# Kernel optimization log

Hardware: AMD Instinct MI355X
Metric: run time of the kernel (lower is better)

The kernel has to match this reference:

```python
import jax, jax.numpy as jnp
import numpy as np

B, T, E, H, S = 4, 4096, 1024, 16, 64
D = E // H  # head_dim = 64
ROPE_BASE = 10000.0


def _rotate_half(x):
    # interleaved rotate: out[..., 2i] = -x[..., 2i+1]; out[..., 2i+1] = x[..., 2i]
    x1 = x[..., ::2]
    x2 = x[..., 1::2]
    return jnp.stack([-x2, x1], axis=-1).reshape(x.shape)


def _rope_cos_sin(t, d):
    inv_freq = 1.0 / (ROPE_BASE ** (jnp.arange(0, d, 2, dtype=jnp.float32) / d))
    freqs = jnp.arange(t, dtype=jnp.float32)[:, None] * inv_freq[None, :]  # [t, d/2]
    emb = jnp.concatenate([freqs, freqs], axis=-1)  # [t, d]
    # broadcast over batch and heads for q/k of shape [b, t, h, d]
    return jnp.cos(emb)[None, :, None, :], jnp.sin(emb)[None, :, None, :]


def setup_inputs() -> dict:
    key = jax.random.key(0)
    ks = jax.random.split(key, 6)
    s = E ** -0.5
    return {
        "x": jax.random.normal(ks[0], (B, T, E), dtype=jnp.float32),
        "Wq": jax.random.normal(ks[1], (E, E), dtype=jnp.float32) * s,
        "Wk": jax.random.normal(ks[2], (E, E), dtype=jnp.float32) * s,
        "Wv": jax.random.normal(ks[3], (E, E), dtype=jnp.float32) * s,
        "Wout": jax.random.normal(ks[4], (E, E), dtype=jnp.float32) * s,
        "slot_keys": jax.random.normal(ks[5], (H, S, D), dtype=jnp.float32) * (D ** -0.5),
    }


def reference(x, Wq, Wk, Wv, Wout, slot_keys):
    b, t, e = x.shape
    h, s_slots, d = slot_keys.shape
    scale = d ** -0.5

    q = (x @ Wq.T).reshape(b, t, h, d)
    k = (x @ Wk.T).reshape(b, t, h, d)
    v = (x @ Wv.T).reshape(b, t, h, d)

    cos, sin = _rope_cos_sin(t, d)
    q = q * cos + _rotate_half(q) * sin
    k = k * cos + _rotate_half(k) * sin

    # write pass: route each token's value into memory slots
    write_logits = jnp.einsum('bthd,hsd->bths', k, slot_keys) * scale
    write_weights = jax.nn.softmax(write_logits, axis=-1)  # write_temperature = 1.0
    slot_state = jnp.einsum('bths,bthd->bshd', write_weights, v) / t

    # read pass: query the slot memory
    read_logits = jnp.einsum('bthd,bshd->bths', q, slot_state) * scale
    read_weights = jax.nn.softmax(read_logits, axis=-1)  # read_temperature = 1.0
    read_out = jnp.einsum('bths,bshd->bthd', read_weights, slot_state)

    return read_out.reshape(b, t, e) @ Wout.T
```

## Files before the change

kernel.cpp:

```cpp
#include <hip/hip_runtime.h>
#include <cstdint>
#include <cstddef>

#define BB 4
#define TT 4096
#define EE 1024
#define HH 16
#define SSLOTS 64
#define DD 64
#define MM (BB*TT)

typedef unsigned short u16;
typedef __attribute__((ext_vector_type(8))) short s16x8;
typedef __attribute__((ext_vector_type(4))) float f32x4;
typedef __attribute__((ext_vector_type(8))) unsigned short us8v;
typedef __attribute__((ext_vector_type(4))) unsigned short us4v;

#define MFMA16(a, b, c) __builtin_amdgcn_mfma_f32_16x16x32_bf16((a), (b), (c), 0, 0, 0)

__device__ __forceinline__ u16 f2bf(float x) {
  union { float f; uint32_t u; } c; c.f = x;
  uint32_t u = c.u;
  u += 0x7fffu + ((u >> 16) & 1u);
  return (u16)(u >> 16);
}

__device__ __forceinline__ float bf2f(u16 x) {
  union { uint32_t u; float f; } c; c.u = ((uint32_t)x) << 16;
  return c.f;
}

__device__ __forceinline__ void async16(const void* g, void* l) {
  auto lp = reinterpret_cast<__attribute__((address_space(3))) void*>(
      reinterpret_cast<uintptr_t>(l));
  auto gp = reinterpret_cast<const __attribute__((address_space(1))) void*>(
      reinterpret_cast<uintptr_t>(g));
  __builtin_amdgcn_global_load_lds(gp, lp, 16, 0, 0);
}

__device__ __forceinline__ us8v rope8(us8v kv, const float* __restrict__ rcp,
                                      const float* __restrict__ rsp) {
  float4 ca = *(const float4*)rcp;
  float4 cb = *(const float4*)(rcp + 4);
  float4 sa = *(const float4*)rsp;
  float4 sb = *(const float4*)(rsp + 4);
  float c[8] = {ca.x, ca.y, ca.z, ca.w, cb.x, cb.y, cb.z, cb.w};
  float s[8] = {sa.x, sa.y, sa.z, sa.w, sb.x, sb.y, sb.z, sb.w};
  float e[8];
#pragma unroll
  for (int m = 0; m < 8; ++m) e[m] = bf2f((u16)kv[m]);
  us8v o;
#pragma unroll
  for (int j = 0; j < 4; ++j) {
    o[2 * j]     = f2bf(e[2 * j] * c[2 * j]     - e[2 * j + 1] * s[2 * j]);
    o[2 * j + 1] = f2bf(e[2 * j + 1] * c[2 * j + 1] + e[2 * j] * s[2 * j + 1]);
  }
  return o;
}

__global__ __launch_bounds__(256) void k_prep(const float* __restrict__ x,
                                              const float* __restrict__ w0,
                                              const float* __restrict__ w1,
                                              const float* __restrict__ w2,
                                              const float* __restrict__ w3,
                                              u16* __restrict__ x16,
                                              u16* __restrict__ dW,
                                              u16* __restrict__ dWo,
                                              float* __restrict__ rc,
                                              float* __restrict__ rs) {
  int bid = blockIdx.x;
  if (bid < 16384) {
    int i = (bid * 256 + threadIdx.x) * 4;
    float4 v = *(const float4*)(x + i);
    us4v o = { f2bf(v.x), f2bf(v.y), f2bf(v.z), f2bf(v.w) };
    *(us4v*)(x16 + i) = o;
  } else if (bid < 16384 + 4096) {
    int bb = bid - 16384;
    int sel = bb >> 10;
    const float* s = (sel == 0) ? w0 : (sel == 1) ? w1 : (sel == 2) ? w2 : w3;
    u16* d = (sel < 3) ? (dW + (size_t)sel * EE * EE) : dWo;
    int i = ((bb & 1023) * 256 + threadIdx.x) * 4;
    float4 v = *(const float4*)(s + i);
    us4v o = { f2bf(v.x), f2bf(v.y), f2bf(v.z), f2bf(v.w) };
    *(us4v*)(d + i) = o;
  } else {
    int i = (bid - 16384 - 4096) * 256 + threadIdx.x;
    int t = i >> 5, f = i & 31;
    double invf = pow(10000.0, -(double)(2 * f) / 64.0);
    double th = fmod((double)t * invf, 6.28318530717958647692528676655900577);
    rc[i] = (float)cos(th);
    rs[i] = (float)sin(th);
  }
}


__device__ __forceinline__ void mm16(f32x4 (&acc)[8][4], const s16x8* a,
                                     const s16x8* b, int ab) {
#pragma unroll
  for (int im = 0; im < 4; ++im)
#pragma unroll
    for (int in = 0; in < 4; ++in)
      acc[ab + im][in] = MFMA16(a[im], b[in], acc[ab + im][in]);
}

__device__ __forceinline__ void gemm256(const u16* __restrict__ A,
                                        const u16* __restrict__ B,
                                        char* smem, f32x4 (&acc)[8][4]) {
  const int tid = threadIdx.x, lane = tid & 63, wave = tid >> 6;
  const int l16 = lane & 15, q4 = lane >> 4;
  const int wrow = (wave >> 2) * 128;
  const int wcol = (wave & 3) * 64;

  const int sr0 = wave * 32 + (lane >> 2);
  const int sr1 = sr0 + 16;
  const int sc  = (lane & 3) * 16;
  const size_t ga0 = (size_t)sr0 * 2048 + (size_t)(sc ^ (((sr0 >> 1) & 3) << 4));
  const size_t ga1 = (size_t)sr1 * 2048 + (size_t)(sc ^ (((sr1 >> 1) & 3) << 4));
  const int lo0 = sr0 * 64 + sc;
  const int lo1 = sr1 * 64 + sc;
  const char* Ab = (const char*)A;
  const char* Bb = (const char*)B;

  int offA[8], offB[4];
#pragma unroll
  for (int f = 0; f < 8; ++f) {
    int r = wrow + f * 16 + l16;
    offA[f] = (r * 64 + q4 * 16) ^ (((r >> 1) & 3) << 4);
  }
#pragma unroll
  for (int f = 0; f < 4; ++f) {
    int r = wcol + f * 16 + l16;
    offB[f] = (r * 64 + q4 * 16) ^ (((r >> 1) & 3) << 4);
  }

#define STG(dst, srcb, kb) do { \
    async16((srcb) + (size_t)(kb) + ga0, (dst) + lo0); \
    async16((srcb) + (size_t)(kb) + ga1, (dst) + lo1); } while (0)

  STG(smem +     0, Ab, 0);
  STG(smem + 32768, Bb, 0);
  STG(smem + 16384, Ab, 64);
  STG(smem + 49152, Bb, 64);
  STG(smem + 65536 +     0, Ab, 128);
  STG(smem + 65536 + 32768, Bb, 128);
  asm volatile("s_waitcnt vmcnt(4)" ::: "memory");
  __builtin_amdgcn_s_barrier();

  for (int tau = 0; tau < 16; ++tau) {
    char* cb = smem + ((tau & 1) << 16);
    char* nb = smem + (((tau + 1) & 1) << 16);
    const char* Ak0 = cb;
    const char* Ak1 = cb + 16384;
    const char* Bk0 = cb + 32768;
    const char* Bk1 = cb + 49152;
    const int kb1 = (tau + 1) << 7;
    const int kb2 = (tau + 2) << 7;
    const bool st1 = tau < 15, st2 = tau < 14;

    s16x8 a[4], b[4];

#pragma unroll
    for (int f = 0; f < 4; ++f) a[f] = *(const s16x8*)(Ak0 + offA[f]);
#pragma unroll
    for (int f = 0; f < 4; ++f) b[f] = *(const s16x8*)(Bk0 + offB[f]);
    if (st1) STG(nb + 16384, Ab, kb1 + 64);
    __builtin_amdgcn_s_barrier();
    asm volatile("s_waitcnt lgkmcnt(0)" ::: "memory");
    __builtin_amdgcn_s_setprio(1);
    mm16(acc, a, b, 0);
    __builtin_amdgcn_s_setprio(0);
    __builtin_amdgcn_s_barrier();

#pragma unroll
    for (int f = 0; f < 4; ++f) a[f] = *(const s16x8*)(Ak0 + offA[4 + f]);
    if (st1) STG(nb + 49152, Bb, kb1 + 64);
    if (st2) asm volatile("s_waitcnt vmcnt(6)" ::: "memory");
    else     asm volatile("s_waitcnt vmcnt(0)" ::: "memory");
    __builtin_amdgcn_s_barrier();
    asm volatile("s_waitcnt lgkmcnt(0)" ::: "memory");
    __builtin_amdgcn_s_setprio(1);
    mm16(acc, a, b, 4);
    __builtin_amdgcn_s_setprio(0);
    __builtin_amdgcn_s_barrier();

#pragma unroll
    for (int f = 0; f < 4; ++f) a[f] = *(const s16x8*)(Ak1 + offA[f]);
#pragma unroll
    for (int f = 0; f < 4; ++f) b[f] = *(const s16x8*)(Bk1 + offB[f]);
    if (st2) STG(cb, Ab, kb2);
    __builtin_amdgcn_s_barrier();
    asm volatile("s_waitcnt lgkmcnt(0)" ::: "memory");
    __builtin_amdgcn_s_setprio(1);
    mm16(acc, a, b, 0);
    __builtin_amdgcn_s_setprio(0);
    __builtin_amdgcn_s_barrier();

#pragma unroll
    for (int f = 0; f < 4; ++f) a[f] = *(const s16x8*)(Ak1 + offA[4 + f]);
    if (st2) STG(cb + 32768, Bb, kb2);
    if (st2) asm volatile("s_waitcnt vmcnt(6)" ::: "memory");
    else     asm volatile("s_waitcnt vmcnt(0)" ::: "memory");
    __builtin_amdgcn_s_barrier();
    asm volatile("s_waitcnt lgkmcnt(0)" ::: "memory");
    __builtin_amdgcn_s_setprio(1);
    mm16(acc, a, b, 4);
    __builtin_amdgcn_s_setprio(0);
    __builtin_amdgcn_s_barrier();
  }
#undef STG
}

__global__ __launch_bounds__(512, 2) void k_gemm_qkv(const u16* __restrict__ A,
                                                     const u16* __restrict__ Bw,
                                                     u16* __restrict__ q16,
                                                     u16* __restrict__ k16,
                                                     u16* __restrict__ v16) {
  __shared__ char smem[131072];
  const int bid = blockIdx.x;
  const int xcd = bid & 7, local = bid >> 3;
  const int mt = xcd * 8 + (local & 7);
  const int nt = local >> 3;
  const int m0 = mt * 256, n0 = nt * 256;

  f32x4 acc[8][4];
#pragma unroll
  for (int i = 0; i < 8; ++i)
#pragma unroll
    for (int j = 0; j < 4; ++j) acc[i][j] = (f32x4){0.f, 0.f, 0.f, 0.f};

  gemm256(A + (size_t)m0 * 1024, Bw + (size_t)n0 * 1024, smem, acc);

  const int tid = threadIdx.x, lane = tid & 63, wave = tid >> 6;
  const int l16 = lane & 15, q4 = lane >> 4;
  const int wrow = (wave >> 2) * 128, wn = (wave & 3) * 64;
  const int which = n0 >> 10;
  const int nbl = n0 & 1023;
  u16* dst = (which == 0) ? q16 : ((which == 1) ? k16 : v16);

#pragma unroll
  for (int im = 0; im < 8; ++im)
#pragma unroll
    for (int in = 0; in < 4; ++in)
#pragma unroll
      for (int reg = 0; reg < 4; ++reg) {
        float v = acc[im][in][reg];
        int m = m0 + wrow + im * 16 + q4 * 4 + reg;
        int nn = nbl + wn + in * 16 + l16;
        int bq = m >> 12, t = m & 4095;
        int h = nn >> 6, d = nn & 63;
        dst[((size_t)(bq * HH + h) * TT + t) * 64 + d] = f2bf(v);
      }
}

__global__ __launch_bounds__(512, 2) void k_gemm_out(const u16* __restrict__ A,
                                                     const u16* __restrict__ Bw,
                                                     float* __restrict__ C) {
  __shared__ char smem[131072];
  const int bid = blockIdx.x;
  const int xcd = bid & 7, local = bid >> 3;
  const int mt = xcd * 8 + (local & 7);
  const int nt = local >> 3;
  const int m0 = mt * 256, n0 = nt * 256;

  f32x4 acc[8][4];
#pragma unroll
  for (int i = 0; i < 8; ++i)
#pragma unroll
    for (int j = 0; j < 4; ++j) acc[i][j] = (f32x4){0.f, 0.f, 0.f, 0.f};

  gemm256(A + (size_t)m0 * 1024, Bw + (size_t)n0 * 1024, smem, acc);

  const int tid = threadIdx.x, lane = tid & 63, wave = tid >> 6;
  const int l16 = lane & 15, q4 = lane >> 4;
  const int wrow = (wave >> 2) * 128, wn = (wave & 3) * 64;
#pragma unroll
  for (int im = 0; im < 8; ++im)
#pragma unroll
    for (int in = 0; in < 4; ++in)
#pragma unroll
      for (int reg = 0; reg < 4; ++reg) {
        int m = m0 + wrow + im * 16 + q4 * 4 + reg;
        int n = n0 + wn + in * 16 + l16;
        C[(size_t)m * 1024 + n] = acc[im][in][reg];
      }
}

__global__ __launch_bounds__(256) void k_stage2(const u16* __restrict__ K16g,
                                                const u16* __restrict__ V16g,
                                                const float* __restrict__ SKg,
                                                const float* __restrict__ rc,
                                                const float* __restrict__ rs,
                                                float* __restrict__ SSb) {
  const int tid = threadIdx.x, lane = tid & 63, wave = tid >> 6;
  const int l16 = lane & 15, q4 = lane >> 4, q8 = q4 * 8;
  const int bh = blockIdx.x >> 4, tb = blockIdx.x & 15;
  const int h = bh & 15;

  __shared__ u16 Ks[128 * 88];
  __shared__ u16 Vs[64 * 136];
  __shared__ u16 SKs[64 * 88];
  u16* ww = Ks;

  const float* skh = SKg + (size_t)h * (SSLOTS * DD);
  for (int i = tid * 4; i < 4096; i += 1024) {
    float4 v = *(const float4*)(skh + i);
    us4v o = { f2bf(v.x), f2bf(v.y), f2bf(v.z), f2bf(v.w) };
    *(us4v*)&SKs[(i >> 6) * 88 + (i & 63)] = o;
  }

  f32x4 a2[4];
#pragma unroll
  for (int in = 0; in < 4; ++in) a2[in] = (f32x4){0.f, 0.f, 0.f, 0.f};

  const int w32 = wave * 32;
  for (int cc = 0; cc < 2; ++cc) {
    const int tg0 = tb * 256 + cc * 128;
    __syncthreads();

    const u16* ks = K16g + ((size_t)bh * TT + tg0) * 64;
    for (int idx = tid; idx < 1024; idx += 256) {
      int t = idx >> 3, p = idx & 7;
      us8v kv = *(const us8v*)(ks + (size_t)t * 64 + p * 8);
      int fi = (tg0 + t) * 32 + ((p * 8) & 31);
      us8v kr = rope8(kv, rc + fi, rs + fi);
      *(us8v*)&Ks[t * 88 + p * 8] = kr;
    }
    const u16* vsrc = V16g + ((size_t)bh * TT + tg0) * 64;
    for (int idx = tid; idx < 1024; idx += 256) {
      int t = idx & 127, dg = idx >> 7;
      us8v vv = *(const us8v*)(vsrc + (size_t)t * 64 + dg * 8);
#pragma unroll
      for (int j = 0; j < 8; ++j) Vs[(dg * 8 + j) * 136 + t] = vv[j];
    }
    __syncthreads();

    f32x4 a1[2][4];
#pragma unroll
    for (int im = 0; im < 2; ++im)
#pragma unroll
      for (int in = 0; in < 4; ++in) a1[im][in] = (f32x4){0.f, 0.f, 0.f, 0.f};
#pragma unroll
    for (int ksx = 0; ksx < 2; ++ksx) {
      s16x8 afr0 = *(const s16x8*)&Ks[(w32 + l16) * 88 + ksx * 32 + q8];
      s16x8 afr1 = *(const s16x8*)&Ks[(w32 + 16 + l16) * 88 + ksx * 32 + q8];
#pragma unroll
      for (int in = 0; in < 4; ++in) {
        s16x8 bfr = *(const s16x8*)&SKs[(in * 16 + l16) * 88 + ksx * 32 + q8];
        a1[0][in] = MFMA16(afr0, bfr, a1[0][in]);
        a1[1][in] = MFMA16(afr1, bfr, a1[1][in]);
      }
    }
    __syncthreads();

#pragma unroll
    for (int im = 0; im < 2; ++im)
#pragma unroll
      for (int reg = 0; reg < 4; ++reg) {
        float v0 = a1[im][0][reg] * 0.125f, v1 = a1[im][1][reg] * 0.125f;
        float v2 = a1[im][2][reg] * 0.125f, v3 = a1[im][3][reg] * 0.125f;
        float mx = fmaxf(fmaxf(v0, v1), fmaxf(v2, v3));
#pragma unroll
        for (int m = 1; m < 16; m <<= 1) mx = fmaxf(mx, __shfl_xor(mx, m));
        float e0 = __expf(v0 - mx), e1 = __expf(v1 - mx);
        float e2 = __expf(v2 - mx), e3 = __expf(v3 - mx);
        float sm = e0 + e1 + e2 + e3;
#pragma unroll
        for (int m = 1; m < 16; m <<= 1) sm += __shfl_xor(sm, m);
        float inv = 1.0f / sm;
        int tl = w32 + im * 16 + q4 * 4 + reg;
        ww[(l16) * 136 + tl]      = f2bf(e0 * inv);
        ww[(16 + l16) * 136 + tl] = f2bf(e1 * inv);
        ww[(32 + l16) * 136 + tl] = f2bf(e2 * inv);
        ww[(48 + l16) * 136 + tl] = f2bf(e3 * inv);
      }
    __syncthreads();

#pragma unroll
    for (int ksx = 0; ksx < 4; ++ksx) {
      s16x8 afr = *(const s16x8*)&ww[(wave * 16 + l16) * 136 + ksx * 32 + q8];
#pragma unroll
      for (int in = 0; in < 4; ++in) {
        s16x8 bfr = *(const s16x8*)&Vs[(in * 16 + l16) * 136 + ksx * 32 + q8];
        a2[in] = MFMA16(afr, bfr, a2[in]);
      }
    }
  }

  const float invT = 1.0f / (float)TT;
#pragma unroll
  for (int in = 0; in < 4; ++in)
#pragma unroll
    for (int reg = 0; reg < 4; ++reg) {
      int s = wave * 16 + q4 * 4 + reg;
      int d = in * 16 + l16;
      atomicAdd(&SSb[(size_t)bh * 4096 + s * 64 + d], a2[in][reg] * invT);
    }
}

__global__ __launch_bounds__(256) void k_stage3(const u16* __restrict__ Q16g,
                                                const float* __restrict__ SSg,
                                                const float* __restrict__ rc,
                                                const float* __restrict__ rs,
                                                u16* __restrict__ RO) {
  const int tid = threadIdx.x, lane = tid & 63, wave = tid >> 6;
  const int l16 = lane & 15, q4 = lane >> 4, q8 = q4 * 8;
  const int bh = blockIdx.x >> 5, ck = blockIdx.x & 31;
  const int b = bh >> 4, h = bh & 15;
  const int tg0 = ck * 128;

  __shared__ u16 Qs[128 * 88];
  __shared__ u16 ss_sd[64 * 88];
  __shared__ u16 ss_ds[64 * 88];
  u16* RWs = Qs;

  const float* ssp = SSg + (size_t)bh * 4096;
  for (int i = tid * 4; i < 4096; i += 1024) {
    float4 v = *(const float4*)(ssp + i);
    us4v o = { f2bf(v.x), f2bf(v.y), f2bf(v.z), f2bf(v.w) };
    int s = i >> 6, d = i & 63;
    *(us4v*)&ss_sd[s * 88 + d] = o;
    ss_ds[(d + 0) * 88 + s] = o[0];
    ss_ds[(d + 1) * 88 + s] = o[1];
    ss_ds[(d + 2) * 88 + s] = o[2];
    ss_ds[(d + 3) * 88 + s] = o[3];
  }
  const u16* qsrc = Q16g + ((size_t)bh * TT + tg0) * 64;
  for (int idx = tid; idx < 1024; idx += 256) {
    int t = idx >> 3, p = idx & 7;
    us8v qv = *(const us8v*)(qsrc + (size_t)t * 64 + p * 8);
    int fi = (tg0 + t) * 32 + ((p * 8) & 31);
    us8v qr = rope8(qv, rc + fi, rs + fi);
    *(us8v*)&Qs[t * 88 + p * 8] = qr;
  }
  __syncthreads();

  const int w32 = wave * 32;
  f32x4 a3[2][4];
#pragma unroll
  for (int i = 0; i < 2; ++i)
#pragma unroll
    for (int j = 0; j < 4; ++j) a3[i][j] = (f32x4){0.f, 0.f, 0.f, 0.f};
#pragma unroll
  for (int ksx = 0; ksx < 2; ++ksx) {
    s16x8 afr[2];
#pragma unroll
    for (int im = 0; im < 2; ++im)
      afr[im] = *(const s16x8*)&Qs[(w32 + im * 16 + l16) * 88 + ksx * 32 + q8];
#pragma unroll
    for (int in = 0; in < 4; ++in) {
      s16x8 bfr = *(const s16x8*)&ss_sd[(in * 16 + l16) * 88 + ksx * 32 + q8];
#pragma unroll
      for (int im = 0; im < 2; ++im) a3[im][in] = MFMA16(afr[im], bfr, a3[im][in]);
    }
  }
  __syncthreads();

#pragma unroll
  for (int im = 0; im < 2; ++im)
#pragma unroll
    for (int reg = 0; reg < 4; ++reg) {
      float v0 = a3[im][0][reg] * 0.125f, v1 = a3[im][1][reg] * 0.125f;
      float v2 = a3[im][2][reg] * 0.125f, v3 = a3[im][3][reg] * 0.125f;
      float mx = fmaxf(fmaxf(v0, v1), fmaxf(v2, v3));
#pragma unroll
      for (int m = 1; m < 16; m <<= 1) mx = fmaxf(mx, __shfl_xor(mx, m));
      float e0 = __expf(v0 - mx), e1 = __expf(v1 - mx);
      float e2 = __expf(v2 - mx), e3 = __expf(v3 - mx);
      float sm = e0 + e1 + e2 + e3;
#pragma unroll
      for (int m = 1; m < 16; m <<= 1) sm += __shfl_xor(sm, m);
      float inv = 1.0f / sm;
      int tl = w32 + im * 16 + q4 * 4 + reg;
      RWs[tl * 88 + l16]      = f2bf(e0 * inv);
      RWs[tl * 88 + 16 + l16] = f2bf(e1 * inv);
      RWs[tl * 88 + 32 + l16] = f2bf(e2 * inv);
      RWs[tl * 88 + 48 + l16] = f2bf(e3 * inv);
    }
  __syncthreads();

  f32x4 a4[2][4];
#pragma unroll
  for (int i = 0; i < 2; ++i)
#pragma unroll
    for (int j = 0; j < 4; ++j) a4[i][j] = (f32x4){0.f, 0.f, 0.f, 0.f};
#pragma unroll
  for (int ksx = 0; ksx < 2; ++ksx) {
    s16x8 afr[2];
#pragma unroll
    for (int im = 0; im < 2; ++im)
      afr[im] = *(const s16x8*)&RWs[(w32 + im * 16 + l16) * 88 + ksx * 32 + q8];
#pragma unroll
    for (int in = 0; in < 4; ++in) {
      s16x8 bfr = *(const s16x8*)&ss_ds[(in * 16 + l16) * 88 + ksx * 32 + q8];
#pragma unroll
      for (int im = 0; im < 2; ++im) a4[im][in] = MFMA16(afr[im], bfr, a4[im][in]);
    }
  }

#pragma unroll
  for (int im = 0; im < 2; ++im)
#pragma unroll
    for (int in = 0; in < 4; ++in)
#pragma unroll
      for (int reg = 0; reg < 4; ++reg) {
        int t = tg0 + w32 + im * 16 + q4 * 4 + reg;
        int d = in * 16 + l16;
        RO[((size_t)b * TT + t) * 1024 + h * 64 + d] = f2bf(a4[im][in][reg]);
      }
}

extern "C" void kernel_launch(void* const* d_in, const int* in_sizes, int n_in,
                              void* d_out, int out_size, void* d_ws, size_t ws_size,
                              hipStream_t stream) {
  const float* x  = (const float*)d_in[0];
  const float* Wq = (const float*)d_in[1];
  const float* Wk = (const float*)d_in[2];
  const float* Wv = (const float*)d_in[3];
  const float* Wo = (const float*)d_in[4];
  const float* SK = (const float*)d_in[5];
  float* out = (float*)d_out;

  char* w = (char*)d_ws;
  u16* x16 = (u16*)w;   w += (size_t)MM * EE * 2;
  u16* W16 = (u16*)w;   w += (size_t)3 * EE * EE * 2;
  u16* Wo16 = (u16*)w;  w += (size_t)EE * EE * 2;
  u16* Q16 = (u16*)w;   w += (size_t)BB * HH * TT * DD * 2;
  u16* K16 = (u16*)w;   w += (size_t)BB * HH * TT * DD * 2;
  u16* V16 = (u16*)w;   w += (size_t)BB * HH * TT * DD * 2;
  float* SSb = (float*)w; w += (size_t)BB * HH * SSLOTS * DD * 4;
  float* rc = (float*)w;  w += (size_t)TT * 32 * 4;
  float* rs = (float*)w;  w += (size_t)TT * 32 * 4;
  u16* RO16 = x16;

  if ((size_t)(w - (char*)d_ws) > ws_size) return;

  k_prep<<<16384 + 4096 + 512, 256, 0, stream>>>(x, Wq, Wk, Wv, Wo, x16, W16, Wo16, rc, rs);

  k_gemm_qkv<<<768, 512, 0, stream>>>(x16, W16, Q16, K16, V16);

  hipMemsetAsync(SSb, 0, (size_t)BB * HH * SSLOTS * DD * 4, stream);
  k_stage2<<<1024, 256, 0, stream>>>(K16, V16, SK, rc, rs, SSb);
  k_stage3<<<2048, 256, 0, stream>>>(Q16, SSb, rc, rs, RO16);

  k_gemm_out<<<256, 512, 0, stream>>>(RO16, Wo16, out);
}
```

Measured before the change: 346.5 us.

## Merge GEMM k-substeps into full-tile MFMA phases and replace atomics with partial-sum reduction

The shared GEMM mainloop now loads all eight A fragments at once and issues 32 MFMAs per phase. This halves the number of barrier-separated phases per k-step and drops the trailing barriers, at the cost of more live registers and both global prefetches being issued together. Stage 2 no longer does float atomicAdd into the slot state. It writes per-block partial slabs, and a new reduce kernel sums them and applies the 1/T scale, which removes the memset and atomic contention but adds a 16 MB workspace round trip and an extra launch.

```diff
diff --git a/kernel.cpp b/kernel.cpp
--- a/kernel.cpp
+++ b/kernel.cpp
@@ -94,13 +94,13 @@
 }
 
 
-__device__ __forceinline__ void mm16(f32x4 (&acc)[8][4], const s16x8* a,
-                                     const s16x8* b, int ab) {
-#pragma unroll
-  for (int im = 0; im < 4; ++im)
+__device__ __forceinline__ void mm32(f32x4 (&acc)[8][4], const s16x8* a,
+                                     const s16x8* b) {
+#pragma unroll
+  for (int im = 0; im < 8; ++im)
 #pragma unroll
     for (int in = 0; in < 4; ++in)
-      acc[ab + im][in] = MFMA16(a[im], b[in], acc[ab + im][in]);
+      acc[im][in] = MFMA16(a[im], b[in], acc[im][in]);
 }
 
 __device__ __forceinline__ void gemm256(const u16* __restrict__ A,
@@ -157,55 +157,39 @@
     const int kb2 = (tau + 2) << 7;
     const bool st1 = tau < 15, st2 = tau < 14;
 
-    s16x8 a[4], b[4];
-
-#pragma unroll
-    for (int f = 0; f < 4; ++f) a[f] = *(const s16x8*)(Ak0 + offA[f]);
+    s16x8 a[8], b[4];
+
+#pragma unroll
+    for (int f = 0; f < 8; ++f) a[f] = *(const s16x8*)(Ak0 + offA[f]);
 #pragma unroll
     for (int f = 0; f < 4; ++f) b[f] = *(const s16x8*)(Bk0 + offB[f]);
-    if (st1) STG(nb + 16384, Ab, kb1 + 64);
-    __builtin_amdgcn_s_barrier();
-    asm volatile("s_waitcnt lgkmcnt(0)" ::: "memory");
-    __builtin_amdgcn_s_setprio(1);
-    mm16(acc, a, b, 0);
-    __builtin_amdgcn_s_setprio(0);
-    __builtin_amdgcn_s_barrier();
-
-#pragma unroll
-    for (int f = 0; f < 4; ++f) a[f] = *(const s16x8*)(Ak0 + offA[4 + f]);
-    if (st1) STG(nb + 49152, Bb, kb1 + 64);
+    if (st1) {
+      STG(nb + 16384, Ab, kb1 + 64);
+      STG(nb + 49152, Bb, kb1 + 64);
+    }
     if (st2) asm volatile("s_waitcnt vmcnt(6)" ::: "memory");
     else     asm volatile("s_waitcnt vmcnt(0)" ::: "memory");
+    asm volatile("s_waitcnt lgkmcnt(0)" ::: "memory");
     __builtin_amdgcn_s_barrier();
-    asm volatile("s_waitcnt lgkmcnt(0)" ::: "memory");
     __builtin_amdgcn_s_setprio(1);
-    mm16(acc, a, b, 4);
+    mm32(acc, a, b);
     __builtin_amdgcn_s_setprio(0);
-    __builtin_amdgcn_s_barrier();
-
-#pragma unroll
-    for (int f = 0; f < 4; ++f) a[f] = *(const s16x8*)(Ak1 + offA[f]);
+
+#pragma unroll
+    for (int f = 0; f < 8; ++f) a[f] = *(const s16x8*)(Ak1 + offA[f]);
 #pragma unroll
     for (int f = 0; f < 4; ++f) b[f] = *(const s16x8*)(Bk1 + offB[f]);
-    if (st2) STG(cb, Ab, kb2);
-    __builtin_amdgcn_s_barrier();
-    asm volatile("s_waitcnt lgkmcnt(0)" ::: "memory");
-    __builtin_amdgcn_s_setprio(1);
-    mm16(acc, a, b, 0);
-    __builtin_amdgcn_s_setprio(0);
-    __builtin_amdgcn_s_barrier();
-
-#pragma unroll
-    for (int f = 0; f < 4; ++f) a[f] = *(const s16x8*)(Ak1 + offA[4 + f]);
-    if (st2) STG(cb + 32768, Bb, kb2);
+    if (st2) {
+      STG(cb, Ab, kb2);
+      STG(cb + 32768, Bb, kb2);
+    }
     if (st2) asm volatile("s_waitcnt vmcnt(6)" ::: "memory");
     else     asm volatile("s_waitcnt vmcnt(0)" ::: "memory");
+    asm volatile("s_waitcnt lgkmcnt(0)" ::: "memory");
     __builtin_amdgcn_s_barrier();
-    asm volatile("s_waitcnt lgkmcnt(0)" ::: "memory");
     __builtin_amdgcn_s_setprio(1);
-    mm16(acc, a, b, 4);
+    mm32(acc, a, b);
     __builtin_amdgcn_s_setprio(0);
-    __builtin_amdgcn_s_barrier();
   }
 #undef STG
 }
@@ -290,7 +274,7 @@
                                                 const float* __restrict__ SKg,
                                                 const float* __restrict__ rc,
                                                 const float* __restrict__ rs,
-                                                float* __restrict__ SSb) {
+                                                float* __restrict__ PS) {
   const int tid = threadIdx.x, lane = tid & 63, wave = tid >> 6;
   const int l16 = lane & 15, q4 = lane >> 4, q8 = q4 * 8;
   const int bh = blockIdx.x >> 4, tb = blockIdx.x & 15;
@@ -386,15 +370,30 @@
     }
   }
 
-  const float invT = 1.0f / (float)TT;
+  float* slab = PS + (size_t)(tb * 64 + bh) * 4096;
 #pragma unroll
   for (int in = 0; in < 4; ++in)
 #pragma unroll
     for (int reg = 0; reg < 4; ++reg) {
       int s = wave * 16 + q4 * 4 + reg;
       int d = in * 16 + l16;
-      atomicAdd(&SSb[(size_t)bh * 4096 + s * 64 + d], a2[in][reg] * invT);
-    }
+      slab[s * 64 + d] = a2[in][reg];
+    }
+}
+
+__global__ __launch_bounds__(256) void k_reduce(const float* __restrict__ PS,
+                                                float* __restrict__ SSb) {
+  const int bh = blockIdx.x, tid = threadIdx.x;
+  const float invT = 1.0f / (float)TT;
+#pragma unroll
+  for (int j = 0; j < 16; ++j) {
+    int i = j * 256 + tid;
+    float acc = 0.f;
+#pragma unroll
+    for (int tb = 0; tb < 16; ++tb)
+      acc += PS[(size_t)(tb * 64 + bh) * 4096 + i];
+    SSb[(size_t)bh * 4096 + i] = acc * invT;
+  }
 }
 
 __global__ __launch_bounds__(256) void k_stage3(const u16* __restrict__ Q16g,
@@ -528,6 +527,7 @@
   u16* K16 = (u16*)w;   w += (size_t)BB * HH * TT * DD * 2;
   u16* V16 = (u16*)w;   w += (size_t)BB * HH * TT * DD * 2;
   float* SSb = (float*)w; w += (size_t)BB * HH * SSLOTS * DD * 4;
+  float* PS = (float*)w;  w += (size_t)16 * 64 * 4096 * 4;
   float* rc = (float*)w;  w += (size_t)TT * 32 * 4;
   float* rs = (float*)w;  w += (size_t)TT * 32 * 4;
   u16* RO16 = x16;
@@ -538,8 +538,8 @@
 
   k_gemm_qkv<<<768, 512, 0, stream>>>(x16, W16, Q16, K16, V16);
 
-  hipMemsetAsync(SSb, 0, (size_t)BB * HH * SSLOTS * DD * 4, stream);
-  k_stage2<<<1024, 256, 0, stream>>>(K16, V16, SK, rc, rs, SSb);
+  k_stage2<<<1024, 256, 0, stream>>>(K16, V16, SK, rc, rs, PS);
+  k_reduce<<<64, 256, 0, stream>>>(PS, SSb);
   k_stage3<<<2048, 256, 0, stream>>>(Q16, SSb, rc, rs, RO16);
 
   k_gemm_out<<<256, 512, 0, stream>>>(RO16, Wo16, out);
```

After: 391.6 us. +13.0%, slower.
